# Optimization experiments

Hardware: AMD Instinct MI355X
Metric: run time of the kernel (lower is better)

## Reference

```python
import jax, jax.numpy as jnp
import numpy as np

B, C, H, W = 2, 64, 128, 128
KH = KW = 3
K = KH * KW
PAD = 1
GROUPS = 8          # conv groups
OFF_GROUPS = 8      # offset groups (offset channels = 2*OFF_GROUPS*K = 144)
NEG_SLOPE = 0.1


def setup_inputs() -> dict:
    key = jax.random.key(0)
    ks = jax.random.split(key, 8)
    s = lambda fan: 1.0 / np.sqrt(fan)
    return {
        "previous_features": jax.random.normal(ks[0], (B, C, H, W), jnp.float32),
        "offsets": jax.random.normal(ks[1], (B, 2 * OFF_GROUPS * K, H, W), jnp.float32),
        "dcn_weight": jax.random.normal(ks[2], (C, C // GROUPS, KH, KW), jnp.float32) * s((C // GROUPS) * K),
        "dcn_bias": jax.random.normal(ks[3], (C,), jnp.float32) * 0.01,
        "w1": jax.random.normal(ks[4], (C, 2 * C, KH, KW), jnp.float32) * s(2 * C * K),
        "b1": jax.random.normal(ks[5], (C,), jnp.float32) * 0.01,
        "w2": jax.random.normal(ks[6], (C, C, KH, KW), jnp.float32) * s(C * K),
        "b2": jax.random.normal(ks[7], (C,), jnp.float32) * 0.01,
    }


def _deform_conv2d(x, offsets, weight, bias):
    """torchvision DeformConv2d, stride=1, pad=1, dil=1, 3x3.
    x: [B,C,H,W]; offsets: [B, 2*og*K, H, W] with per-tap (dy, dx) pairs.
    """
    b, c, h, w = x.shape
    og = offsets.shape[1] // (2 * K)
    cg_off = c // og
    # [B, og, K, 2, H, W] -> dy, dx each [B, og, K, H, W]
    off = offsets.reshape(b, og, K, 2, h, w)
    dy, dx = off[:, :, :, 0], off[:, :, :, 1]
    # base sampling grid per kernel tap
    by = jnp.repeat(jnp.arange(KH), KW).astype(x.dtype)   # [K]
    bx = jnp.tile(jnp.arange(KW), KH).astype(x.dtype)     # [K]
    py = jnp.arange(h, dtype=x.dtype)[None, None, None, :, None] - PAD \
         + by[None, None, :, None, None] + dy              # [B,og,K,H,W]
    px = jnp.arange(w, dtype=x.dtype)[None, None, None, None, :] - PAD \
         + bx[None, None, :, None, None] + dx

    y0 = jnp.floor(py); x0 = jnp.floor(px)
    wy = py - y0;       wx = px - x0
    y0i = y0.astype(jnp.int32); x0i = x0.astype(jnp.int32)

    xg = x.reshape(b, og, cg_off, h * w)  # channel-grouped, flat spatial

    def samp(yi, xi):
        valid = (yi >= 0) & (yi < h) & (xi >= 0) & (xi < w)
        idx = jnp.clip(yi, 0, h - 1) * w + jnp.clip(xi, 0, w - 1)   # [B,og,K,H,W]
        v = jnp.take_along_axis(xg, idx.reshape(b, og, 1, K * h * w), axis=-1)
        v = v.reshape(b, og, cg_off, K, h, w)
        return v * valid[:, :, None].astype(x.dtype)

    v00 = samp(y0i,     x0i)
    v01 = samp(y0i,     x0i + 1)
    v10 = samp(y0i + 1, x0i)
    v11 = samp(y0i + 1, x0i + 1)
    wy_ = wy[:, :, None]; wx_ = wx[:, :, None]  # [B,og,1,K,H,W]
    sampled = (v00 * (1 - wy_) * (1 - wx_) + v01 * (1 - wy_) * wx_
               + v10 * wy_ * (1 - wx_) + v11 * wy_ * wx_)   # [B,og,Cg,K,H,W]

    g = c // weight.shape[1]
    cg = c // g
    cols = sampled.reshape(b, g, cg, K, h, w)                # channel order preserved
    w_g = weight.reshape(g, cg, cg, K)                       # [g, cout/g, cin/g, K]
    out = jnp.einsum('goik,bgikhw->bgohw', w_g, cols).reshape(b, c, h, w)
    return out + bias[None, :, None, None]


def _conv3x3(x, w, b):
    out = jax.lax.conv_general_dilated(
        x, w, window_strides=(1, 1), padding='SAME',
        dimension_numbers=('NCHW', 'OIHW', 'NCHW'))
    return out + b[None, :, None, None]


def _lrelu(x):
    return jnp.where(x >= 0, x, NEG_SLOPE * x)


def reference(previous_features, offsets, dcn_weight, dcn_bias, w1, b1, w2, b2):
    aligned = _deform_conv2d(previous_features, offsets, dcn_weight, dcn_bias)
    r = jnp.concatenate([aligned, previous_features], axis=1)
    r = _lrelu(_conv3x3(r, w1, b1))
    r = _lrelu(_conv3x3(r, w2, b2))
    return aligned + r
```

## Files before the change

kernel.cpp:

```cpp
#include <hip/hip_runtime.h>
#include <stdint.h>

typedef _Float16 h2 __attribute__((ext_vector_type(2)));
typedef _Float16 half8 __attribute__((ext_vector_type(8)));
typedef float f32x4 __attribute__((ext_vector_type(4)));
typedef unsigned int u32x4 __attribute__((ext_vector_type(4)));
typedef unsigned int u32x2 __attribute__((ext_vector_type(2)));

constexpr int B_ = 2, C_ = 64, H_ = 128, W_ = 128, HW_ = H_ * W_;
constexpr float NEG_SLOPE = 0.1f;

__device__ inline unsigned short f2h(float f) {
    _Float16 h = (_Float16)f;
    union { _Float16 h; unsigned short s; } c; c.h = h; return c.s;
}
__device__ inline float h2f(unsigned short s) {
    union { unsigned short s; _Float16 h; } c; c.s = s; return (float)c.h;
}
__device__ inline h2 u2h2(unsigned u) {
    union { unsigned u; h2 h; } c; c.u = u; return c.h;
}
__device__ inline unsigned h22u(h2 h) {
    union { unsigned u; h2 h; } c; c.h = h; return c.u;
}

__global__ __launch_bounds__(256) void prep_pack(
    const float* __restrict__ x, const float* __restrict__ dw,
    unsigned short* __restrict__ x_g, unsigned short* __restrict__ dwr)
{
    __shared__ unsigned short t[64][72];
    const int bx = blockIdx.x;
    const int tid = threadIdx.x;

    if (bx < 512) {
        const int b  = bx >> 8;
        const int p0 = (bx & 255) * 64;
#pragma unroll
        for (int u = tid; u < 4096; u += 256) {
            const int c = u >> 6, pp = u & 63;
            t[pp][c ^ ((pp & 7) << 3)] = f2h(x[((size_t)b * 64 + c) * HW_ + p0 + pp]);
        }
        __syncthreads();
#pragma unroll
        for (int u = tid; u < 512; u += 256) {
            const int g = u >> 6, pp = u & 63;
            const u32x4 v = *(const u32x4*)&t[pp][(g ^ (pp & 7)) * 8];
            *(u32x4*)(x_g + (((size_t)b * 8 + g) * HW_ + p0 + pp) * 8) = v;
        }
        return;
    }

    const int idx = (bx - 512) * 256 + tid;
    if (idx < 8 * 3 * 64 * 8) {
        const int g = idx / 1536, r = idx - g * 1536;
        const int c = r / 512, r2 = r - c * 512;
        const int lane = r2 >> 3, j = r2 & 7;
        const int hi = lane >> 4, l15 = lane & 15;
        const int tp = c * 4 + hi;
        float v = 0.f;
        if (l15 < 8 && tp < 9) v = dw[((g * 8 + l15) * 8 + j) * 9 + tp];
        dwr[idx] = f2h(v);
    }
}

__global__ __launch_bounds__(256, 5) void dcn_mfma(
    const unsigned short* __restrict__ x_g,
    const float* __restrict__ off,
    const unsigned short* __restrict__ dwr,
    const float* __restrict__ bias,
    unsigned short* __restrict__ al_cl,
    const float* __restrict__ w1, const float* __restrict__ w2,
    unsigned short* __restrict__ w1a, unsigned short* __restrict__ w2a)
{
    const int tid  = threadIdx.x;
    const int bx0  = blockIdx.x;

    if (bx0 >= 4096) {
        const int idx = (bx0 - 4096) * 256 + tid;
        if (idx < 64 * 1152) {
            const int ici = idx & 31, t2 = idx >> 5;
            const int oc = t2 & 63, ks = t2 >> 6;
            const int icc = ks / 9, tap = ks - icc * 9;
            w1a[idx] = f2h(w1[(oc * 128 + icc * 32 + ici) * 9 + tap]);
        }
        if (idx < 64 * 576) {
            const int ici = idx & 31, t2 = idx >> 5;
            const int oc = t2 & 63, ks = t2 >> 6;
            const int icc = ks / 9, tap = ks - icc * 9;
            w2a[idx] = f2h(w2[(oc * 64 + icc * 32 + ici) * 9 + tap]);
        }
        return;
    }

    const int wv   = tid >> 6;
    const int lane = tid & 63;
    const int hi   = lane >> 4;
    const int l15  = lane & 15;
    const int bx   = ((bx0 & 7) << 9) | (bx0 >> 3);
    const int tile = bx & 2047;
    const int gq   = bx >> 11;
    const int b    = tile >> 10;
    const int p    = ((tile & 1023) << 4) + l15;
    const int h    = p >> 7;
    const int w    = p & (W_ - 1);

    const int g = wv + gq * 4;
    const unsigned short* xg = x_g + ((size_t)b * 8 + g) * HW_ * 8;
    const float* offp = off + ((size_t)b * 144 + g * 18) * HW_ + p;

    float dy0 = offp[(hi * 2 + 0) * HW_];
    float dx0 = offp[(hi * 2 + 1) * HW_];
    float dy1 = offp[((4 + hi) * 2 + 0) * HW_];
    float dx1 = offp[((4 + hi) * 2 + 1) * HW_];
    float dy2 = 0.f, dx2 = 0.f;
    if (hi == 0) { dy2 = offp[16 * HW_]; dx2 = offp[17 * HW_]; }

    u32x4 cr[3][4];
    float fw[3][4];
#pragma unroll
    for (int s = 0; s < 3; ++s) {
        const bool active = (s < 2) || (hi == 0);
        if (active) {
            const int t = s * 4 + hi;
            const float dy = (s == 0) ? dy0 : (s == 1) ? dy1 : dy2;
            const float dx = (s == 0) ? dx0 : (s == 1) ? dx1 : dx2;
            const float py = (float)(h - 1 + t / 3) + dy;
            const float px = (float)(w - 1 + t % 3) + dx;
            const float y0f = floorf(py), x0f = floorf(px);
            const int y0 = (int)y0f, x0 = (int)x0f;
            const int y1 = y0 + 1,  x1 = x0 + 1;
            const float wy = py - y0f, wx = px - x0f;

            const bool vy0 = (unsigned)y0 < (unsigned)H_;
            const bool vy1 = (unsigned)y1 < (unsigned)H_;
            const bool vx0 = (unsigned)x0 < (unsigned)W_;
            const bool vx1 = (unsigned)x1 < (unsigned)W_;

            fw[s][0] = (vy0 && vx0) ? (1.f - wy) * (1.f - wx) : 0.f;
            fw[s][1] = (vy0 && vx1) ? (1.f - wy) * wx         : 0.f;
            fw[s][2] = (vy1 && vx0) ? wy * (1.f - wx)         : 0.f;
            fw[s][3] = (vy1 && vx1) ? wy * wx                 : 0.f;

            const int cy0 = min(max(y0, 0), H_ - 1);
            const int cy1 = min(max(y1, 0), H_ - 1);
            const int cx0 = min(max(x0, 0), W_ - 1);
            const int cx1 = min(max(x1, 0), W_ - 1);

            cr[s][0] = *(const u32x4*)(xg + (size_t)(cy0 * W_ + cx0) * 8);
            cr[s][1] = *(const u32x4*)(xg + (size_t)(cy0 * W_ + cx1) * 8);
            cr[s][2] = *(const u32x4*)(xg + (size_t)(cy1 * W_ + cx0) * 8);
            cr[s][3] = *(const u32x4*)(xg + (size_t)(cy1 * W_ + cx1) * 8);
        }
    }

    f32x4 acc = (f32x4){0.f, 0.f, 0.f, 0.f};
#pragma unroll
    for (int s = 0; s < 3; ++s) {
        half8 bfr = (half8){0, 0, 0, 0, 0, 0, 0, 0};
        if ((s < 2) || (hi == 0)) {
            const h2 f0 = (h2){(_Float16)fw[s][0], (_Float16)fw[s][0]};
            const h2 f1 = (h2){(_Float16)fw[s][1], (_Float16)fw[s][1]};
            const h2 f2 = (h2){(_Float16)fw[s][2], (_Float16)fw[s][2]};
            const h2 f3 = (h2){(_Float16)fw[s][3], (_Float16)fw[s][3]};
            unsigned rq[4];
#pragma unroll
            for (int q = 0; q < 4; ++q) {
                h2 r = u2h2(cr[s][0][q]) * f0;
                r = u2h2(cr[s][1][q]) * f1 + r;
                r = u2h2(cr[s][2][q]) * f2 + r;
                r = u2h2(cr[s][3][q]) * f3 + r;
                rq[q] = h22u(r);
            }
            bfr = *(const half8*)rq;
        }
        const half8 afr = *(const half8*)(dwr + ((g * 3 + s) * 64 + lane) * 8);
        acc = __builtin_amdgcn_mfma_f32_16x16x32_f16(afr, bfr, acc, 0, 0, 0);
    }

    if (hi < 2) {
        unsigned short o4[4];
#pragma unroll
        for (int r = 0; r < 4; ++r)
            o4[r] = f2h(acc[r] + bias[g * 8 + hi * 4 + r]);
        *(u32x2*)(al_cl + ((size_t)b * HW_ + p) * 64 + g * 8 + hi * 4) = *(u32x2*)o4;
    }
}

template <int CIN, bool FINAL>
__global__ __launch_bounds__(256) void conv_mfma(
    const unsigned short* __restrict__ in0,
    const unsigned short* __restrict__ x_g,
    const unsigned short* __restrict__ wa,
    const float* __restrict__ bias,
    const unsigned short* __restrict__ resid_cl,
    float* __restrict__ outf,
    unsigned short* __restrict__ outb)
{
    constexpr int NICC = CIN / 32;
    __shared__ unsigned short b_lds[2][3 * 66 * 32];

    const int tid  = threadIdx.x;
    const int lane = tid & 63;
    const int l15  = lane & 15;
    const int hi   = lane >> 4;
    const int wp   = (tid >> 6) & 1;
    const int wo   = tid >> 7;
    const int flat = blockIdx.x;
    const int nf   = ((flat & 7) << 6) | (flat >> 3);
    const int b    = nf >> 8;
    const int rem  = nf & 255;
    const int row  = rem >> 1;
    const int ct   = rem & 1;
    const int col0 = ct * 64;
    const int oc0w = wo * 32;

    f32x4 acc[2][2];
#pragma unroll
    for (int fm = 0; fm < 2; ++fm)
#pragma unroll
        for (int fn = 0; fn < 2; ++fn)
            acc[fm][fn] = (f32x4){0.f, 0.f, 0.f, 0.f};

    u32x4 sreg[4];

    auto ldregs = [&](int icc) {
#pragma unroll
        for (int t = 0; t < 4; ++t) {
            const int u = tid + t * 256;
            u32x4 v = (u32x4){0u, 0u, 0u, 0u};
            if (u < 792) {
                const int icq = u & 3, rc = u >> 2;
                const int ri = rc / 66, hc = rc - ri * 66;
                const int gr = row + ri - 1, gc = col0 + hc - 1;
                if ((unsigned)gr < 128u && (unsigned)gc < 128u) {
                    const int pix = gr * 128 + gc;
                    if (CIN == 64 || icc < 2)
                        v = *(const u32x4*)(in0 + ((size_t)b * HW_ + pix) * 64
                                             + icc * 32 + icq * 8);
                    else {
                        const int g = (icc - 2) * 4 + icq;
                        v = *(const u32x4*)(x_g + (((size_t)b * 8 + g) * HW_ + pix) * 8);
                    }
                }
            }
            sreg[t] = v;
        }
    };

    auto dswrite = [&](int buf) {
        char* bp = (char*)b_lds[buf];
#pragma unroll
        for (int t = 0; t < 4; ++t) {
            const int u = tid + t * 256;
            if (u < 792) {
                const int icq = u & 3, rc = u >> 2;
                const int hc = rc % 66;
                *(u32x4*)(bp + ((rc * 64 + icq * 16) ^ ((hc & 7) << 4))) = sreg[t];
            }
        }
    };

    auto compute = [&](int icc, int buf) {
        const char* bp = (const char*)b_lds[buf];
#pragma unroll
        for (int tap = 0; tap < 9; ++tap) {
            const int tr = tap / 3, tc = tap - tr * 3;
            half8 af[2], bfr[2];
#pragma unroll
            for (int fm = 0; fm < 2; ++fm)
                af[fm] = *(const half8*)(wa +
                    ((size_t)((icc * 9 + tap) * 64) + oc0w + fm * 16 + l15) * 32 + hi * 8);
#pragma unroll
            for (int fn = 0; fn < 2; ++fn) {
                const int hcol = wp * 32 + fn * 16 + l15 + tc;
                bfr[fn] = *(const half8*)(bp +
                    (((tr * 66 + hcol) * 64 + hi * 16) ^ ((hcol & 7) << 4)));
            }
#pragma unroll
            for (int fm = 0; fm < 2; ++fm)
#pragma unroll
                for (int fn = 0; fn < 2; ++fn)
                    acc[fm][fn] = __builtin_amdgcn_mfma_f32_16x16x32_f16(
                        af[fm], bfr[fn], acc[fm][fn], 0, 0, 0);
        }
    };

    ldregs(0);
    dswrite(0);
    __syncthreads();
#pragma unroll
    for (int icc = 0; icc < NICC; ++icc) {
        if (icc + 1 < NICC) ldregs(icc + 1);
        compute(icc, icc & 1);
        if (icc + 1 < NICC) {
            dswrite((icc + 1) & 1);
            __syncthreads();
        }
    }

    const int prow = row * 128 + col0 + wp * 32;
    if (!FINAL) {
#pragma unroll
        for (int fm = 0; fm < 2; ++fm)
#pragma unroll
            for (int fn = 0; fn < 2; ++fn) {
                const int px = prow + fn * 16 + l15;
                unsigned short o4[4];
#pragma unroll
                for (int r = 0; r < 4; ++r) {
                    const int oc = oc0w + fm * 16 + hi * 4 + r;
                    float v = acc[fm][fn][r] + bias[oc];
                    v = (v >= 0.f) ? v : NEG_SLOPE * v;
                    o4[r] = f2h(v);
                }
                *(u32x2*)(outb + ((size_t)b * HW_ + px) * 64 + oc0w + fm * 16 + hi * 4)
                    = *(u32x2*)o4;
            }
    } else {
#pragma unroll
        for (int fm = 0; fm < 2; ++fm)
#pragma unroll
            for (int fn = 0; fn < 2; ++fn) {
                const int px = prow + fn * 16 + l15;
                const size_t gp = (size_t)b * HW_ + px;
                u32x2 alv = *(const u32x2*)(resid_cl + gp * 64 + oc0w + fm * 16 + hi * 4);
                unsigned short alu[4];
                *(u32x2*)alu = alv;
#pragma unroll
                for (int r = 0; r < 4; ++r) {
                    const int oc = oc0w + fm * 16 + hi * 4 + r;
                    float v = acc[fm][fn][r] + bias[oc];
                    v = (v >= 0.f) ? v : NEG_SLOPE * v;
                    v += h2f(alu[r]);
                    outf[((size_t)b * C_ + oc) * HW_ + px] = v;
                }
            }
    }
}

extern "C" void kernel_launch(void* const* d_in, const int* in_sizes, int n_in,
                              void* d_out, int out_size, void* d_ws, size_t ws_size,
                              hipStream_t stream) {
    const float* x   = (const float*)d_in[0];
    const float* off = (const float*)d_in[1];
    const float* dw  = (const float*)d_in[2];
    const float* db  = (const float*)d_in[3];
    const float* w1  = (const float*)d_in[4];
    const float* b1  = (const float*)d_in[5];
    const float* w2  = (const float*)d_in[6];
    const float* b2  = (const float*)d_in[7];
    float* out = (float*)d_out;

    unsigned short* al_cl = (unsigned short*)d_ws;
    unsigned short* x_g   = al_cl + (size_t)B_ * HW_ * 64;
    unsigned short* t1_cl = x_g + (size_t)B_ * HW_ * 64;
    unsigned short* w1a   = t1_cl + (size_t)B_ * HW_ * 64;
    unsigned short* w2a   = w1a + 64 * 1152;
    unsigned short* dwr   = w2a + 64 * 576;

    prep_pack<<<512 + 48, 256, 0, stream>>>(x, dw, x_g, dwr);
    dcn_mfma<<<4096 + 288, 256, 0, stream>>>(x_g, off, dwr, db, al_cl,
                                             w1, w2, w1a, w2a);
    conv_mfma<128, false><<<512, 256, 0, stream>>>(
        al_cl, x_g, w1a, b1, nullptr, nullptr, t1_cl);
    conv_mfma<64, true><<<512, 256, 0, stream>>>(
        t1_cl, nullptr, w2a, b2, al_cl, out, nullptr);
}
```

Measured before the change: 51.37 us.

## Split conv1 input channels and overlap the x half with the DCN kernel

```diff
diff --git a/kernel.cpp b/kernel.cpp
--- a/kernel.cpp
+++ b/kernel.cpp
@@ -24,9 +24,158 @@
     union { unsigned u; h2 h; } c; c.h = h; return c.u;
 }
 
+template <int ICC_BASE, int NICC, int MODE>
+__device__ __forceinline__ void conv_body(int flat, int tid,
+    const unsigned short* __restrict__ in0,
+    const unsigned short* __restrict__ x_g,
+    const unsigned short* __restrict__ wa,
+    const float* __restrict__ bias,
+    float* __restrict__ part,
+    const unsigned short* __restrict__ resid_cl,
+    float* __restrict__ outf,
+    unsigned short* __restrict__ outb)
+{
+    __shared__ unsigned short b_lds[2][3 * 66 * 32];
+
+    const int lane = tid & 63;
+    const int l15  = lane & 15;
+    const int hi   = lane >> 4;
+    const int wp   = (tid >> 6) & 1;
+    const int wo   = tid >> 7;
+    const int nf   = ((flat & 7) << 6) | (flat >> 3);
+    const int b    = nf >> 8;
+    const int rem  = nf & 255;
+    const int row  = rem >> 1;
+    const int ct   = rem & 1;
+    const int col0 = ct * 64;
+    const int oc0w = wo * 32;
+
+    f32x4 acc[2][2];
+#pragma unroll
+    for (int fm = 0; fm < 2; ++fm)
+#pragma unroll
+        for (int fn = 0; fn < 2; ++fn)
+            acc[fm][fn] = (f32x4){0.f, 0.f, 0.f, 0.f};
+
+    u32x4 sreg[4];
+
+    auto ldregs = [&](int icc) {
+#pragma unroll
+        for (int t = 0; t < 4; ++t) {
+            const int u = tid + t * 256;
+            u32x4 v = (u32x4){0u, 0u, 0u, 0u};
+            if (u < 792) {
+                const int icq = u & 3, rc = u >> 2;
+                const int ri = rc / 66, hc = rc - ri * 66;
+                const int gr = row + ri - 1, gc = col0 + hc - 1;
+                if ((unsigned)gr < 128u && (unsigned)gc < 128u) {
+                    const int pix = gr * 128 + gc;
+                    if (icc < 2)
+                        v = *(const u32x4*)(in0 + ((size_t)b * HW_ + pix) * 64
+                                             + icc * 32 + icq * 8);
+                    else {
+                        const int g = (icc - 2) * 4 + icq;
+                        v = *(const u32x4*)(x_g + (((size_t)b * 8 + g) * HW_ + pix) * 8);
+                    }
+                }
+            }
+            sreg[t] = v;
+        }
+    };
+
+    auto dswrite = [&](int buf) {
+        char* bp = (char*)b_lds[buf];
+#pragma unroll
+        for (int t = 0; t < 4; ++t) {
+            const int u = tid + t * 256;
+            if (u < 792) {
+                const int icq = u & 3, rc = u >> 2;
+                const int hc = rc % 66;
+                *(u32x4*)(bp + ((rc * 64 + icq * 16) ^ ((hc & 7) << 4))) = sreg[t];
+            }
+        }
+    };
+
+    auto compute = [&](int icc, int buf) {
+        const char* bp = (const char*)b_lds[buf];
+#pragma unroll
+        for (int tap = 0; tap < 9; ++tap) {
+            const int tr = tap / 3, tc = tap - tr * 3;
+            half8 af[2], bfr[2];
+#pragma unroll
+            for (int fm = 0; fm < 2; ++fm)
+                af[fm] = *(const half8*)(wa +
+                    ((size_t)((icc * 9 + tap) * 64) + oc0w + fm * 16 + l15) * 32 + hi * 8);
+#pragma unroll
+            for (int fn = 0; fn < 2; ++fn) {
+                const int hcol = wp * 32 + fn * 16 + l15 + tc;
+                bfr[fn] = *(const half8*)(bp +
+                    (((tr * 66 + hcol) * 64 + hi * 16) ^ ((hcol & 7) << 4)));
+            }
+#pragma unroll
+            for (int fm = 0; fm < 2; ++fm)
+#pragma unroll
+                for (int fn = 0; fn < 2; ++fn)
+                    acc[fm][fn] = __builtin_amdgcn_mfma_f32_16x16x32_f16(
+                        af[fm], bfr[fn], acc[fm][fn], 0, 0, 0);
+        }
+    };
+
+    ldregs(ICC_BASE);
+    dswrite(0);
+    __syncthreads();
+#pragma unroll
+    for (int ic = 0; ic < NICC; ++ic) {
+        if (ic + 1 < NICC) ldregs(ICC_BASE + ic + 1);
+        compute(ICC_BASE + ic, ic & 1);
+        if (ic + 1 < NICC) {
+            dswrite((ic + 1) & 1);
+            __syncthreads();
+        }
+    }
+
+    const int prow = row * 128 + col0 + wp * 32;
+#pragma unroll
+    for (int fm = 0; fm < 2; ++fm)
+#pragma unroll
+        for (int fn = 0; fn < 2; ++fn) {
+            const int px = prow + fn * 16 + l15;
+            const size_t gp = (size_t)b * HW_ + px;
+            const size_t cidx = gp * 64 + oc0w + fm * 16 + hi * 4;
+            if (MODE == 0) {
+                *(f32x4*)&part[cidx] = acc[fm][fn];
+            } else if (MODE == 1) {
+                const f32x4 pv = *(const f32x4*)&part[cidx];
+                unsigned short o4[4];
+#pragma unroll
+                for (int r = 0; r < 4; ++r) {
+                    const int oc = oc0w + fm * 16 + hi * 4 + r;
+                    float v = acc[fm][fn][r] + pv[r] + bias[oc];
+                    v = (v >= 0.f) ? v : NEG_SLOPE * v;
+                    o4[r] = f2h(v);
+                }
+                *(u32x2*)(outb + cidx) = *(u32x2*)o4;
+            } else {
+                u32x2 alv = *(const u32x2*)(resid_cl + cidx);
+                unsigned short alu[4];
+                *(u32x2*)alu = alv;
+#pragma unroll
+                for (int r = 0; r < 4; ++r) {
+                    const int oc = oc0w + fm * 16 + hi * 4 + r;
+                    float v = acc[fm][fn][r] + bias[oc];
+                    v = (v >= 0.f) ? v : NEG_SLOPE * v;
+                    v += h2f(alu[r]);
+                    outf[((size_t)b * C_ + oc) * HW_ + px] = v;
+                }
+            }
+        }
+}
+
 __global__ __launch_bounds__(256) void prep_pack(
     const float* __restrict__ x, const float* __restrict__ dw,
-    unsigned short* __restrict__ x_g, unsigned short* __restrict__ dwr)
+    const float* __restrict__ w1,
+    unsigned short* __restrict__ x_g, unsigned short* __restrict__ dwr,
+    unsigned short* __restrict__ w1a)
 {
     __shared__ unsigned short t[64][72];
     const int bx = blockIdx.x;
@@ -51,6 +200,12 @@
     }
 
     const int idx = (bx - 512) * 256 + tid;
+    if (idx < 64 * 1152) {
+        const int ici = idx & 31, t2 = idx >> 5;
+        const int oc = t2 & 63, ks = t2 >> 6;
+        const int icc = ks / 9, tap = ks - icc * 9;
+        w1a[idx] = f2h(w1[(oc * 128 + icc * 32 + ici) * 9 + tap]);
+    }
     if (idx < 8 * 3 * 64 * 8) {
         const int g = idx / 1536, r = idx - g * 1536;
         const int c = r / 512, r2 = r - c * 512;
@@ -69,20 +224,21 @@
     const unsigned short* __restrict__ dwr,
     const float* __restrict__ bias,
     unsigned short* __restrict__ al_cl,
-    const float* __restrict__ w1, const float* __restrict__ w2,
-    unsigned short* __restrict__ w1a, unsigned short* __restrict__ w2a)
+    const float* __restrict__ w2,
+    const unsigned short* __restrict__ w1a,
+    unsigned short* __restrict__ w2a,
+    float* __restrict__ part)
 {
     const int tid  = threadIdx.x;
     const int bx0  = blockIdx.x;
 
+    if (bx0 >= 4240) {
+        conv_body<2, 2, 0>(bx0 - 4240, tid, nullptr, x_g, w1a, nullptr,
+                           part, nullptr, nullptr, nullptr);
+        return;
+    }
     if (bx0 >= 4096) {
         const int idx = (bx0 - 4096) * 256 + tid;
-        if (idx < 64 * 1152) {
-            const int ici = idx & 31, t2 = idx >> 5;
-            const int oc = t2 & 63, ks = t2 >> 6;
-            const int icc = ks / 9, tap = ks - icc * 9;
-            w1a[idx] = f2h(w1[(oc * 128 + icc * 32 + ici) * 9 + tap]);
-        }
         if (idx < 64 * 576) {
             const int ici = idx & 31, t2 = idx >> 5;
             const int oc = t2 & 63, ks = t2 >> 6;
@@ -186,156 +342,22 @@
     }
 }
 
-template <int CIN, bool FINAL>
-__global__ __launch_bounds__(256) void conv_mfma(
-    const unsigned short* __restrict__ in0,
-    const unsigned short* __restrict__ x_g,
-    const unsigned short* __restrict__ wa,
-    const float* __restrict__ bias,
-    const unsigned short* __restrict__ resid_cl,
-    float* __restrict__ outf,
-    unsigned short* __restrict__ outb)
-{
-    constexpr int NICC = CIN / 32;
-    __shared__ unsigned short b_lds[2][3 * 66 * 32];
-
-    const int tid  = threadIdx.x;
-    const int lane = tid & 63;
-    const int l15  = lane & 15;
-    const int hi   = lane >> 4;
-    const int wp   = (tid >> 6) & 1;
-    const int wo   = tid >> 7;
-    const int flat = blockIdx.x;
-    const int nf   = ((flat & 7) << 6) | (flat >> 3);
-    const int b    = nf >> 8;
-    const int rem  = nf & 255;
-    const int row  = rem >> 1;
-    const int ct   = rem & 1;
-    const int col0 = ct * 64;
-    const int oc0w = wo * 32;
-
-    f32x4 acc[2][2];
-#pragma unroll
-    for (int fm = 0; fm < 2; ++fm)
-#pragma unroll
-        for (int fn = 0; fn < 2; ++fn)
-            acc[fm][fn] = (f32x4){0.f, 0.f, 0.f, 0.f};
-
-    u32x4 sreg[4];
-
-    auto ldregs = [&](int icc) {
-#pragma unroll
-        for (int t = 0; t < 4; ++t) {
-            const int u = tid + t * 256;
-            u32x4 v = (u32x4){0u, 0u, 0u, 0u};
-            if (u < 792) {
-                const int icq = u & 3, rc = u >> 2;
-                const int ri = rc / 66, hc = rc - ri * 66;
-                const int gr = row + ri - 1, gc = col0 + hc - 1;
-                if ((unsigned)gr < 128u && (unsigned)gc < 128u) {
-                    const int pix = gr * 128 + gc;
-                    if (CIN == 64 || icc < 2)
-                        v = *(const u32x4*)(in0 + ((size_t)b * HW_ + pix) * 64
-                                             + icc * 32 + icq * 8);
-                    else {
-                        const int g = (icc - 2) * 4 + icq;
-                        v = *(const u32x4*)(x_g + (((size_t)b * 8 + g) * HW_ + pix) * 8);
-                    }
-                }
-            }
-            sreg[t] = v;
-        }
-    };
-
-    auto dswrite = [&](int buf) {
-        char* bp = (char*)b_lds[buf];
-#pragma unroll
-        for (int t = 0; t < 4; ++t) {
-            const int u = tid + t * 256;
-            if (u < 792) {
-                const int icq = u & 3, rc = u >> 2;
-                const int hc = rc % 66;
-                *(u32x4*)(bp + ((rc * 64 + icq * 16) ^ ((hc & 7) << 4))) = sreg[t];
-            }
-        }
-    };
-
-    auto compute = [&](int icc, int buf) {
-        const char* bp = (const char*)b_lds[buf];
-#pragma unroll
-        for (int tap = 0; tap < 9; ++tap) {
-            const int tr = tap / 3, tc = tap - tr * 3;
-            half8 af[2], bfr[2];
-#pragma unroll
-            for (int fm = 0; fm < 2; ++fm)
-                af[fm] = *(const half8*)(wa +
-                    ((size_t)((icc * 9 + tap) * 64) + oc0w + fm * 16 + l15) * 32 + hi * 8);
-#pragma unroll
-            for (int fn = 0; fn < 2; ++fn) {
-                const int hcol = wp * 32 + fn * 16 + l15 + tc;
-                bfr[fn] = *(const half8*)(bp +
-                    (((tr * 66 + hcol) * 64 + hi * 16) ^ ((hcol & 7) << 4)));
-            }
-#pragma unroll
-            for (int fm = 0; fm < 2; ++fm)
-#pragma unroll
-                for (int fn = 0; fn < 2; ++fn)
-                    acc[fm][fn] = __builtin_amdgcn_mfma_f32_16x16x32_f16(
-                        af[fm], bfr[fn], acc[fm][fn], 0, 0, 0);
-        }
-    };
-
-    ldregs(0);
-    dswrite(0);
-    __syncthreads();
-#pragma unroll
-    for (int icc = 0; icc < NICC; ++icc) {
-        if (icc + 1 < NICC) ldregs(icc + 1);
-        compute(icc, icc & 1);
-        if (icc + 1 < NICC) {
-            dswrite((icc + 1) & 1);
-            __syncthreads();
-        }
-    }
-
-    const int prow = row * 128 + col0 + wp * 32;
-    if (!FINAL) {
-#pragma unroll
-        for (int fm = 0; fm < 2; ++fm)
-#pragma unroll
-            for (int fn = 0; fn < 2; ++fn) {
-                const int px = prow + fn * 16 + l15;
-                unsigned short o4[4];
-#pragma unroll
-                for (int r = 0; r < 4; ++r) {
-                    const int oc = oc0w + fm * 16 + hi * 4 + r;
-                    float v = acc[fm][fn][r] + bias[oc];
-                    v = (v >= 0.f) ? v : NEG_SLOPE * v;
-                    o4[r] = f2h(v);
-                }
-                *(u32x2*)(outb + ((size_t)b * HW_ + px) * 64 + oc0w + fm * 16 + hi * 4)
-                    = *(u32x2*)o4;
-            }
-    } else {
-#pragma unroll
-        for (int fm = 0; fm < 2; ++fm)
-#pragma unroll
-            for (int fn = 0; fn < 2; ++fn) {
-                const int px = prow + fn * 16 + l15;
-                const size_t gp = (size_t)b * HW_ + px;
-                u32x2 alv = *(const u32x2*)(resid_cl + gp * 64 + oc0w + fm * 16 + hi * 4);
-                unsigned short alu[4];
-                *(u32x2*)alu = alv;
-#pragma unroll
-                for (int r = 0; r < 4; ++r) {
-                    const int oc = oc0w + fm * 16 + hi * 4 + r;
-                    float v = acc[fm][fn][r] + bias[oc];
-                    v = (v >= 0.f) ? v : NEG_SLOPE * v;
-                    v += h2f(alu[r]);
-                    outf[((size_t)b * C_ + oc) * HW_ + px] = v;
-                }
-            }
-    }
+__global__ __launch_bounds__(256) void conv1a_k(
+    const unsigned short* __restrict__ al_cl,
+    const unsigned short* __restrict__ w1a, const float* __restrict__ b1,
+    float* __restrict__ part, unsigned short* __restrict__ t1_cl)
+{
+    conv_body<0, 2, 1>(blockIdx.x, threadIdx.x, al_cl, nullptr, w1a, b1,
+                       part, nullptr, nullptr, t1_cl);
+}
+
+__global__ __launch_bounds__(256) void conv2_k(
+    const unsigned short* __restrict__ t1_cl,
+    const unsigned short* __restrict__ w2a, const float* __restrict__ b2,
+    const unsigned short* __restrict__ al_cl, float* __restrict__ out)
+{
+    conv_body<0, 2, 2>(blockIdx.x, threadIdx.x, t1_cl, nullptr, w2a, b2,
+                       nullptr, al_cl, out, nullptr);
 }
 
 extern "C" void kernel_launch(void* const* d_in, const int* in_sizes, int n_in,
@@ -357,12 +379,11 @@
     unsigned short* w1a   = t1_cl + (size_t)B_ * HW_ * 64;
     unsigned short* w2a   = w1a + 64 * 1152;
     unsigned short* dwr   = w2a + 64 * 576;
-
-    prep_pack<<<512 + 48, 256, 0, stream>>>(x, dw, x_g, dwr);
-    dcn_mfma<<<4096 + 288, 256, 0, stream>>>(x_g, off, dwr, db, al_cl,
-                                             w1, w2, w1a, w2a);
-    conv_mfma<128, false><<<512, 256, 0, stream>>>(
-        al_cl, x_g, w1a, b1, nullptr, nullptr, t1_cl);
-    conv_mfma<64, true><<<512, 256, 0, stream>>>(
-        t1_cl, nullptr, w2a, b2, al_cl, out, nullptr);
-}
+    float*          part  = (float*)(dwr + 8 * 3 * 64 * 8 + 64);
+
+    prep_pack<<<512 + 288, 256, 0, stream>>>(x, dw, w1, x_g, dwr, w1a);
+    dcn_mfma<<<4096 + 144 + 512, 256, 0, stream>>>(x_g, off, dwr, db, al_cl,
+                                                   w2, w1a, w2a, part);
+    conv1a_k<<<512, 256, 0, stream>>>(al_cl, w1a, b1, part, t1_cl);
+    conv2_k<<<512, 256, 0, stream>>>(t1_cl, w2a, b2, al_cl, out);
+}
```

New measurement: 56.79 us. +10.6%, slower.
